# Performance work log

Hardware: AMD Instinct MI355X
Metric: run time of the kernel (lower is better)

The kernel has to match this reference:

```python
import jax, jax.numpy as jnp
import numpy as np

N_HEAD = 16


def setup_inputs() -> dict:
    key = jax.random.key(0)
    k0, k1, k2, k3 = jax.random.split(key, 4)
    B, T, C = 2, 2048, 1024
    scale = 0.02
    x = jax.random.normal(k0, (B, T, C), dtype=jnp.float32)
    W_attn = jax.random.normal(k1, (C, 3 * C), dtype=jnp.float32) * scale
    b_attn = jnp.zeros((3 * C,), dtype=jnp.float32)
    W_proj = jax.random.normal(k2, (C, C), dtype=jnp.float32) * scale
    b_proj = jnp.zeros((C,), dtype=jnp.float32)
    return {"x": x, "W_attn": W_attn, "b_attn": b_attn, "W_proj": W_proj, "b_proj": b_proj}


def reference(x, W_attn, b_attn, W_proj, b_proj):
    B, T, C = x.shape
    H = N_HEAD
    hd = C // H
    # fused qkv projection
    qkv = x @ W_attn + b_attn                      # [B, T, 3C]
    q, k, v = jnp.split(qkv, 3, axis=-1)
    q = q.reshape(B, T, H, hd).transpose(0, 2, 1, 3)  # [B, H, T, hd]
    k = k.reshape(B, T, H, hd).transpose(0, 2, 1, 3)
    v = v.reshape(B, T, H, hd).transpose(0, 2, 1, 3)
    # scaled dot-product attention with causal mask (past_kv=None -> seq_len == T)
    att = jnp.einsum('bhqd,bhkd->bhqk', q, k) / jnp.sqrt(jnp.float32(hd))
    causal = jnp.tril(jnp.ones((T, T), dtype=bool))  # [T, T]
    att = jnp.where(causal[None, None, :, :], att, jnp.float32(-jnp.inf))
    att = jax.nn.softmax(att, axis=-1)
    y = jnp.einsum('bhqk,bhkd->bhqd', att, v)        # [B, H, T, hd]
    y = y.transpose(0, 2, 1, 3).reshape(B, T, C)
    y = y @ W_proj + b_proj
    return (y, k, v)  # (output, present_k, present_v)
```

## Files before the change

kernel.cpp:

```cpp
#include <hip/hip_runtime.h>
#include <hip/hip_bf16.h>

typedef __bf16 bf16;
typedef __bf16 bf16x8 __attribute__((ext_vector_type(8)));
typedef float f32x4 __attribute__((ext_vector_type(4)));
typedef unsigned int u32;

#define MFMA_BF16(a, b, c) __builtin_amdgcn_mfma_f32_16x16x32_bf16((a), (b), (c), 0, 0, 0)

#define SEQ_T 2048
#define DIM_C 1024

__device__ inline void gload16(const void* g, void* l) {
  __builtin_amdgcn_global_load_lds((const __attribute__((address_space(1))) u32*)g,
                                   (__attribute__((address_space(3))) u32*)l, 16, 0, 0);
}

__device__ inline bf16x8 cvt8f(const f32x4 a, const f32x4 b) {
  bf16x8 r;
  r[0] = (bf16)a[0]; r[1] = (bf16)a[1]; r[2] = (bf16)a[2]; r[3] = (bf16)a[3];
  r[4] = (bf16)b[0]; r[5] = (bf16)b[1]; r[6] = (bf16)b[2]; r[7] = (bf16)b[3];
  return r;
}

__global__ __launch_bounds__(256) void prep_kernel(
    const float* __restrict__ x, const float* __restrict__ Wa,
    const float* __restrict__ Wp, bf16* __restrict__ xbf,
    bf16* __restrict__ wat, bf16* __restrict__ wpt) {
  const int tid = threadIdx.x;
  const int bid = blockIdx.x;
  if (bid < 2048) {
    const size_t i = ((size_t)bid * 256 + tid) * 8;
    *(bf16x8*)(xbf + i) = cvt8f(*(const f32x4*)(x + i), *(const f32x4*)(x + i + 4));
  } else if (bid < 3584) {
    const int cid = (bid - 2048) * 256 + tid;
    const int kg = cid / 3072, n = cid - kg * 3072;
    bf16x8 r;
#pragma unroll
    for (int j = 0; j < 8; j++) r[j] = (bf16)Wa[(size_t)(kg * 8 + j) * 3072 + n];
    *(bf16x8*)(wat + (size_t)cid * 8) = r;
  } else {
    const int cid = (bid - 3584) * 256 + tid;
    const int kg = cid >> 10, n = cid & 1023;
    bf16x8 r;
#pragma unroll
    for (int j = 0; j < 8; j++) r[j] = (bf16)Wp[(size_t)(kg * 8 + j) * 1024 + n];
    *(bf16x8*)(wpt + (size_t)cid * 8) = r;
  }
}

__global__ __launch_bounds__(256) void img_kernel(
    const float* __restrict__ K, const float* __restrict__ V,
    bf16* __restrict__ kimg, bf16* __restrict__ vimg) {
  const int gid = blockIdx.x * 256 + threadIdx.x;
  const int ka = gid >> 3, h8 = gid & 7;
  const size_t src = (size_t)ka * 64 + h8 * 8;
  const bf16x8 rk = cvt8f(*(const f32x4*)(K + src), *(const f32x4*)(K + src + 4));
  const bf16x8 rv = cvt8f(*(const f32x4*)(V + src), *(const f32x4*)(V + src + 4));
  const size_t tb = (size_t)(ka & ~63) * 64;
  const int kl = ka & 63, k7 = ka & 7, cq = (ka >> 3) & 7;
  *(bf16x8*)(kimg + tb + kl * 64 + ((h8 ^ k7) * 8)) = rk;
#pragma unroll
  for (int e = 0; e < 8; e++) {
    const int hr = h8 * 8 + e;
    vimg[tb + hr * 64 + ((cq ^ (hr & 7)) * 8) + k7] = rv[e];
  }
}

template <int MODE, int BM, int BK>
__global__ __launch_bounds__(256) void gemm_kernel(
    const bf16* __restrict__ A, const bf16* __restrict__ Wt,
    const float* __restrict__ bias, float* __restrict__ out0,
    float* __restrict__ out1, bf16* __restrict__ bq, int M, int N, int K) {
  constexpr int MI = BM / 32;
  constexpr int CA = BM * BK / 2048;
  constexpr int CB = BK / 16;
  constexpr int RPC = 512 / BK;
  constexpr int EPB = BK / 8;
  __shared__ bf16 As[2][BM * BK];
  __shared__ bf16 Bt[2][128 * BK];

  const int tid = threadIdx.x;
  const int wid = tid >> 6, lane = tid & 63;
  const int quad = lane >> 4, l16 = lane & 15;
  const int wm = (wid >> 1) * (BM / 2), wn = (wid & 1) * 64;
  const int m0 = blockIdx.y * BM, n0 = blockIdx.x * 128;
  const int lr = lane / EPB, lks = lane % EPB;

  const f32x4 zero = {0.f, 0.f, 0.f, 0.f};
  f32x4 acc[MI][4];
#pragma unroll
  for (int i = 0; i < MI; i++)
#pragma unroll
    for (int j = 0; j < 4; j++) acc[i][j] = zero;

  auto stage = [&](int buf, int kk) {
#pragma unroll
    for (int p = 0; p < CA; p++) {
      const int c = wid * CA + p;
      gload16(A + (size_t)(m0 + c * RPC + lr) * K + kk + lks * 8,
              (bf16*)As[buf] + c * 512);
    }
#pragma unroll
    for (int p = 0; p < CB; p++) {
      const int c = wid * CB + p;
      gload16(Wt + ((size_t)((kk >> 3) + lks) * N + n0 + c * RPC + lr) * 8,
              (bf16*)Bt[buf] + c * 512);
    }
  };

  const int nt = K / BK;
  stage(0, 0);
  __syncthreads();
  int cur = 0;
  for (int t = 0; t < nt; t++) {
    if (t + 1 < nt) stage(cur ^ 1, (t + 1) * BK);
#pragma unroll
    for (int kb = 0; kb < BK / 32; kb++) {
      bf16x8 af[MI], bfr[4];
#pragma unroll
      for (int i = 0; i < MI; i++)
        af[i] = *(const bf16x8*)&As[cur][(wm + i * 16 + l16) * BK + kb * 32 + quad * 8];
#pragma unroll
      for (int j = 0; j < 4; j++)
        bfr[j] = *(const bf16x8*)&Bt[cur][(wn + j * 16 + l16) * BK + kb * 32 + quad * 8];
#pragma unroll
      for (int i = 0; i < MI; i++)
#pragma unroll
        for (int j = 0; j < 4; j++)
          acc[i][j] = MFMA_BF16(af[i], bfr[j], acc[i][j]);
    }
    __syncthreads();
    cur ^= 1;
  }

#pragma unroll
  for (int i = 0; i < MI; i++) {
#pragma unroll
    for (int j = 0; j < 4; j++) {
      const int col = n0 + wn + j * 16 + l16;
      const float bv = bias[col];
#pragma unroll
      for (int r = 0; r < 4; r++) {
        const int gm = m0 + wm + i * 16 + quad * 4 + r;
        const float v = acc[i][j][r] + bv;
        if (MODE == 0) {
          out0[(size_t)gm * N + col] = v;
        } else {
          const int which = col >> 10, c = col & 1023;
          const int h = c >> 6, d = c & 63;
          const int b = gm >> 11, t = gm & (SEQ_T - 1);
          const size_t idx = ((size_t)(b * 16 + h) * SEQ_T + t) * 64 + d;
          if (which == 0) {
            bq[idx] = (bf16)(v * 0.18033688f);
          } else if (which == 1) {
            out0[idx] = v;
          } else {
            out1[idx] = v;
          }
        }
      }
    }
  }
}

__global__ __launch_bounds__(512) void attn_kernel(
    const bf16* __restrict__ Qbf, const bf16* __restrict__ Kimg,
    const bf16* __restrict__ Vimg, bf16* __restrict__ Y) {
  __shared__ bf16 Ks[2][4096];
  __shared__ bf16 Vt[2][4096];
  __shared__ bf16 Ps[8 * 1024];

  const int tid = threadIdx.x;
  const int wid = tid >> 6, lane = tid & 63;
  const int quad = lane >> 4, l16 = lane & 15;

  const int qt = (blockIdx.y < 16) ? ((int)gridDim.x - 1 - (int)blockIdx.x)
                                   : (int)blockIdx.x;
  const int bh = blockIdx.y;
  const int q0 = qt * 128;
  const int b = bh >> 4, h = bh & 15;

  const bf16* qp = Qbf + (size_t)bh * SEQ_T * 64;
  const bf16* kp = Kimg + (size_t)bh * SEQ_T * 64;
  const bf16* vp = Vimg + (size_t)bh * SEQ_T * 64;

  bf16x8 aq[2];
#pragma unroll
  for (int ks = 0; ks < 2; ks++)
    aq[ks] = *(const bf16x8*)(qp + (size_t)(q0 + wid * 16 + l16) * 64 + ks * 32 + quad * 8);

  bf16x8 bones;
#pragma unroll
  for (int j = 0; j < 8; j++) bones[j] = (bf16)1.0f;

  const f32x4 zero = {0.f, 0.f, 0.f, 0.f};
  f32x4 oacc[4], lacc;
  lacc = zero;
#pragma unroll
  for (int t = 0; t < 4; t++) oacc[t] = zero;

  const int last = 2 * qt + 1;

  auto stage = [&](int buf, int t) {
    const size_t tb = (size_t)t * 4096 + (size_t)tid * 8;
    bf16* wb = &Ks[buf][wid << 9];
    gload16(kp + tb, wb);
    gload16(vp + tb, &Vt[buf][wid << 9]);
  };

  stage(0, 0);
  __syncthreads();

  for (int it = 0; it <= last; ++it) {
    const int cur = it & 1;
    if (it < last) stage(cur ^ 1, it + 1);

    const bool skip = (it == last) && (wid < 4);
    const bool dm = (it == 2 * qt && wid < 4) || (it == last && wid >= 4);

    if (!skip) {
      f32x4 sa[4];
#pragma unroll
      for (int nt = 0; nt < 4; nt++) {
        const int row = nt * 16 + l16, r7 = l16 & 7;
        const bf16x8 bk0 = *(const bf16x8*)&Ks[cur][row * 64 + ((quad ^ r7) * 8)];
        const bf16x8 bk1 = *(const bf16x8*)&Ks[cur][row * 64 + (((quad + 4) ^ r7) * 8)];
        f32x4 s = MFMA_BF16(aq[0], bk0, zero);
        sa[nt] = MFMA_BF16(aq[1], bk1, s);
      }
      if (dm) {
#pragma unroll
        for (int nt = 0; nt < 4; nt++) {
          const int col = it * 64 + nt * 16 + l16;
#pragma unroll
          for (int r = 0; r < 4; r++) {
            const int row = q0 + wid * 16 + quad * 4 + r;
            if (col > row) sa[nt][r] = -1e30f;
          }
        }
      }
      bf16* pwb = &Ps[wid * 1024];
#pragma unroll
      for (int nt = 0; nt < 4; nt++) {
#pragma unroll
        for (int r = 0; r < 4; r++) {
          const int pr = quad * 4 + r;
          pwb[pr * 64 + (((2 * nt + (l16 >> 3)) ^ (pr & 7)) * 8) + (l16 & 7)] =
              (bf16)exp2f(sa[nt][r]);
        }
      }
      bf16x8 ap[2];
#pragma unroll
      for (int ks = 0; ks < 2; ks++)
        ap[ks] = *(const bf16x8*)&pwb[l16 * 64 + (((ks * 4 + quad) ^ (l16 & 7)) * 8)];
      lacc = MFMA_BF16(ap[0], bones, lacc);
      lacc = MFMA_BF16(ap[1], bones, lacc);
#pragma unroll
      for (int nt = 0; nt < 4; nt++) {
        const int hr = nt * 16 + l16, h7 = l16 & 7;
#pragma unroll
        for (int ks = 0; ks < 2; ks++) {
          const bf16x8 bv = *(const bf16x8*)&Vt[cur][hr * 64 + (((ks * 4 + quad) ^ h7) * 8)];
          oacc[nt] = MFMA_BF16(ap[ks], bv, oacc[nt]);
        }
      }
    }
    __syncthreads();
  }

  float inv[4];
#pragma unroll
  for (int r = 0; r < 4; r++) inv[r] = 1.f / lacc[r];
#pragma unroll
  for (int nt = 0; nt < 4; nt++) {
#pragma unroll
    for (int r = 0; r < 4; r++) {
      const int row = q0 + wid * 16 + quad * 4 + r;
      const int col = h * 64 + nt * 16 + l16;
      Y[((size_t)(b * SEQ_T + row)) * DIM_C + col] = (bf16)(oacc[nt][r] * inv[r]);
    }
  }
}

extern "C" void kernel_launch(void* const* d_in, const int* in_sizes, int n_in,
                              void* d_out, int out_size, void* d_ws, size_t ws_size,
                              hipStream_t stream) {
  (void)in_sizes; (void)n_in; (void)out_size; (void)ws_size;
  const float* x = (const float*)d_in[0];
  const float* W_attn = (const float*)d_in[1];
  const float* b_attn = (const float*)d_in[2];
  const float* W_proj = (const float*)d_in[3];
  const float* b_proj = (const float*)d_in[4];

  float* out = (float*)d_out;
  float* y_out = out;
  float* k_out = out + (size_t)4194304;
  float* v_out = out + (size_t)8388608;
  bf16* qbf = (bf16*)d_out;
  bf16* kimg = (bf16*)d_out + 4194304;
  bf16* y_att = (bf16*)d_in[0];
  bf16* vimg = (bf16*)d_in[0] + 4194304;
  bf16* xbf = (bf16*)d_ws;
  bf16* wat = xbf + 4194304;
  bf16* wpt = wat + 3145728;

  prep_kernel<<<4096, 256, 0, stream>>>(x, W_attn, W_proj, xbf, wat, wpt);
  gemm_kernel<1, 128, 32><<<dim3(3072 / 128, 4096 / 128), 256, 0, stream>>>(
      xbf, wat, b_attn, k_out, v_out, qbf, 4096, 3072, 1024);
  img_kernel<<<2048, 256, 0, stream>>>(k_out, v_out, kimg, vimg);
  attn_kernel<<<dim3(SEQ_T / 128, 32), 512, 0, stream>>>(qbf, kimg, vimg, y_att);
  gemm_kernel<0, 64, 64><<<dim3(1024 / 128, 4096 / 64), 256, 0, stream>>>(
      y_att, wpt, b_proj, y_out, nullptr, nullptr, 4096, 1024, 1024);
}
```

Before: 207.2 us.

## Use atomic work queue for attention and transpose V through LDS

The attention kernel becomes persistent. Each block pulls (query-tile, head) jobs from a global atomic counter, ordered longest causal tile first, to balance the uneven causal workload across CUs. The img kernel now resets the counter and splits into two parts: V blocks build the transposed, swizzled tile in shared memory and then write it out coalesced, and K blocks keep the old path. This adds an atomic and a barrier per job and reuses the workspace head as the counter.

```diff
diff --git a/kernel.cpp b/kernel.cpp
--- a/kernel.cpp
+++ b/kernel.cpp
@@ -51,19 +51,36 @@
 
 __global__ __launch_bounds__(256) void img_kernel(
     const float* __restrict__ K, const float* __restrict__ V,
-    bf16* __restrict__ kimg, bf16* __restrict__ vimg) {
-  const int gid = blockIdx.x * 256 + threadIdx.x;
-  const int ka = gid >> 3, h8 = gid & 7;
-  const size_t src = (size_t)ka * 64 + h8 * 8;
-  const bf16x8 rk = cvt8f(*(const f32x4*)(K + src), *(const f32x4*)(K + src + 4));
-  const bf16x8 rv = cvt8f(*(const f32x4*)(V + src), *(const f32x4*)(V + src + 4));
-  const size_t tb = (size_t)(ka & ~63) * 64;
-  const int kl = ka & 63, k7 = ka & 7, cq = (ka >> 3) & 7;
-  *(bf16x8*)(kimg + tb + kl * 64 + ((h8 ^ k7) * 8)) = rk;
-#pragma unroll
-  for (int e = 0; e < 8; e++) {
-    const int hr = h8 * 8 + e;
-    vimg[tb + hr * 64 + ((cq ^ (hr & 7)) * 8) + k7] = rv[e];
+    bf16* __restrict__ kimg, bf16* __restrict__ vimg, int* __restrict__ cnt) {
+  const int tid = threadIdx.x;
+  const int bid = blockIdx.x;
+  if (bid == 0 && tid == 0) *cnt = 0;
+  if (bid < 1024) {
+    __shared__ bf16 vt[4096];
+    const size_t tb = (size_t)bid * 4096;
+    const int key = tid >> 2, cs = (tid & 3) * 16;
+    const int k7 = key & 7, cq = (key >> 3) & 7;
+    const float* vsrc = V + tb + (size_t)key * 64 + cs;
+#pragma unroll
+    for (int jj = 0; jj < 16; jj += 4) {
+      const f32x4 v4 = *(const f32x4*)(vsrc + jj);
+#pragma unroll
+      for (int e = 0; e < 4; e++) {
+        const int hr = cs + jj + e;
+        vt[hr * 64 + ((cq ^ (hr & 7)) * 8) + k7] = (bf16)v4[e];
+      }
+    }
+    __syncthreads();
+    *(bf16x8*)(vimg + tb + tid * 16) = *(const bf16x8*)&vt[tid * 16];
+    *(bf16x8*)(vimg + tb + tid * 16 + 8) = *(const bf16x8*)&vt[tid * 16 + 8];
+  } else {
+    const int gid = (bid - 1024) * 256 + tid;
+    const int ka = gid >> 3, h8 = gid & 7;
+    const size_t src = (size_t)ka * 64 + h8 * 8;
+    const bf16x8 rk = cvt8f(*(const f32x4*)(K + src), *(const f32x4*)(K + src + 4));
+    const size_t tb = (size_t)(ka & ~63) * 64;
+    const int kl = ka & 63, k7 = ka & 7;
+    *(bf16x8*)(kimg + tb + kl * 64 + ((h8 ^ k7) * 8)) = rk;
   }
 }
 
@@ -166,119 +183,123 @@
 
 __global__ __launch_bounds__(512) void attn_kernel(
     const bf16* __restrict__ Qbf, const bf16* __restrict__ Kimg,
-    const bf16* __restrict__ Vimg, bf16* __restrict__ Y) {
+    const bf16* __restrict__ Vimg, bf16* __restrict__ Y, int* __restrict__ cnt) {
   __shared__ bf16 Ks[2][4096];
   __shared__ bf16 Vt[2][4096];
   __shared__ bf16 Ps[8 * 1024];
+  __shared__ int js;
 
   const int tid = threadIdx.x;
   const int wid = tid >> 6, lane = tid & 63;
   const int quad = lane >> 4, l16 = lane & 15;
 
-  const int qt = (blockIdx.y < 16) ? ((int)gridDim.x - 1 - (int)blockIdx.x)
-                                   : (int)blockIdx.x;
-  const int bh = blockIdx.y;
-  const int q0 = qt * 128;
-  const int b = bh >> 4, h = bh & 15;
-
-  const bf16* qp = Qbf + (size_t)bh * SEQ_T * 64;
-  const bf16* kp = Kimg + (size_t)bh * SEQ_T * 64;
-  const bf16* vp = Vimg + (size_t)bh * SEQ_T * 64;
-
-  bf16x8 aq[2];
-#pragma unroll
-  for (int ks = 0; ks < 2; ks++)
-    aq[ks] = *(const bf16x8*)(qp + (size_t)(q0 + wid * 16 + l16) * 64 + ks * 32 + quad * 8);
-
   bf16x8 bones;
 #pragma unroll
   for (int j = 0; j < 8; j++) bones[j] = (bf16)1.0f;
-
   const f32x4 zero = {0.f, 0.f, 0.f, 0.f};
-  f32x4 oacc[4], lacc;
-  lacc = zero;
-#pragma unroll
-  for (int t = 0; t < 4; t++) oacc[t] = zero;
-
-  const int last = 2 * qt + 1;
-
-  auto stage = [&](int buf, int t) {
-    const size_t tb = (size_t)t * 4096 + (size_t)tid * 8;
-    bf16* wb = &Ks[buf][wid << 9];
-    gload16(kp + tb, wb);
-    gload16(vp + tb, &Vt[buf][wid << 9]);
-  };
-
-  stage(0, 0);
-  __syncthreads();
-
-  for (int it = 0; it <= last; ++it) {
-    const int cur = it & 1;
-    if (it < last) stage(cur ^ 1, it + 1);
-
-    const bool skip = (it == last) && (wid < 4);
-    const bool dm = (it == 2 * qt && wid < 4) || (it == last && wid >= 4);
-
-    if (!skip) {
-      f32x4 sa[4];
-#pragma unroll
-      for (int nt = 0; nt < 4; nt++) {
-        const int row = nt * 16 + l16, r7 = l16 & 7;
-        const bf16x8 bk0 = *(const bf16x8*)&Ks[cur][row * 64 + ((quad ^ r7) * 8)];
-        const bf16x8 bk1 = *(const bf16x8*)&Ks[cur][row * 64 + (((quad + 4) ^ r7) * 8)];
-        f32x4 s = MFMA_BF16(aq[0], bk0, zero);
-        sa[nt] = MFMA_BF16(aq[1], bk1, s);
+
+  for (;;) {
+    if (tid == 0) js = atomicAdd(cnt, 1);
+    __syncthreads();
+    const int j = js;
+    if (j >= 512) break;
+    const int qt = 15 - (j >> 5), bh = j & 31;
+    const int q0 = qt * 128;
+    const int b = bh >> 4, h = bh & 15;
+
+    const bf16* qp = Qbf + (size_t)bh * SEQ_T * 64;
+    const bf16* kp = Kimg + (size_t)bh * SEQ_T * 64;
+    const bf16* vp = Vimg + (size_t)bh * SEQ_T * 64;
+
+    bf16x8 aq[2];
+#pragma unroll
+    for (int ks = 0; ks < 2; ks++)
+      aq[ks] = *(const bf16x8*)(qp + (size_t)(q0 + wid * 16 + l16) * 64 + ks * 32 + quad * 8);
+
+    f32x4 oacc[4], lacc;
+    lacc = zero;
+#pragma unroll
+    for (int t = 0; t < 4; t++) oacc[t] = zero;
+
+    const int last = 2 * qt + 1;
+
+    auto stage = [&](int buf, int t) {
+      const size_t tb = (size_t)t * 4096 + (size_t)tid * 8;
+      gload16(kp + tb, &Ks[buf][wid << 9]);
+      gload16(vp + tb, &Vt[buf][wid << 9]);
+    };
+
+    stage(0, 0);
+    __syncthreads();
+
+    for (int it = 0; it <= last; ++it) {
+      const int cur = it & 1;
+      if (it < last) stage(cur ^ 1, it + 1);
+
+      const bool skip = (it == last) && (wid < 4);
+      const bool dm = (it == 2 * qt && wid < 4) || (it == last && wid >= 4);
+
+      if (!skip) {
+        f32x4 sa[4];
+#pragma unroll
+        for (int nt = 0; nt < 4; nt++) {
+          const int row = nt * 16 + l16, r7 = l16 & 7;
+          const bf16x8 bk0 = *(const bf16x8*)&Ks[cur][row * 64 + ((quad ^ r7) * 8)];
+          const bf16x8 bk1 = *(const bf16x8*)&Ks[cur][row * 64 + (((quad + 4) ^ r7) * 8)];
+          f32x4 s = MFMA_BF16(aq[0], bk0, zero);
+          sa[nt] = MFMA_BF16(aq[1], bk1, s);
+        }
+        if (dm) {
+#pragma unroll
+          for (int nt = 0; nt < 4; nt++) {
+            const int col = it * 64 + nt * 16 + l16;
+#pragma unroll
+            for (int r = 0; r < 4; r++) {
+              const int row = q0 + wid * 16 + quad * 4 + r;
+              if (col > row) sa[nt][r] = -1e30f;
+            }
+          }
+        }
+        bf16* pwb = &Ps[wid * 1024];
+#pragma unroll
+        for (int nt = 0; nt < 4; nt++) {
+#pragma unroll
+          for (int r = 0; r < 4; r++) {
+            const int pr = quad * 4 + r;
+            pwb[pr * 64 + (((2 * nt + (l16 >> 3)) ^ (pr & 7)) * 8) + (l16 & 7)] =
+                (bf16)exp2f(sa[nt][r]);
+          }
+        }
+        bf16x8 ap[2];
+#pragma unroll
+        for (int ks = 0; ks < 2; ks++)
+          ap[ks] = *(const bf16x8*)&pwb[l16 * 64 + (((ks * 4 + quad) ^ (l16 & 7)) * 8)];
+        lacc = MFMA_BF16(ap[0], bones, lacc);
+        lacc = MFMA_BF16(ap[1], bones, lacc);
+#pragma unroll
+        for (int nt = 0; nt < 4; nt++) {
+          const int hr = nt * 16 + l16, h7 = l16 & 7;
+#pragma unroll
+          for (int ks = 0; ks < 2; ks++) {
+            const bf16x8 bv = *(const bf16x8*)&Vt[cur][hr * 64 + (((ks * 4 + quad) ^ h7) * 8)];
+            oacc[nt] = MFMA_BF16(ap[ks], bv, oacc[nt]);
+          }
+        }
       }
-      if (dm) {
-#pragma unroll
-        for (int nt = 0; nt < 4; nt++) {
-          const int col = it * 64 + nt * 16 + l16;
-#pragma unroll
-          for (int r = 0; r < 4; r++) {
-            const int row = q0 + wid * 16 + quad * 4 + r;
-            if (col > row) sa[nt][r] = -1e30f;
-          }
-        }
+      __syncthreads();
+    }
+
+    float inv[4];
+#pragma unroll
+    for (int r = 0; r < 4; r++) inv[r] = 1.f / lacc[r];
+#pragma unroll
+    for (int nt = 0; nt < 4; nt++) {
+#pragma unroll
+      for (int r = 0; r < 4; r++) {
+        const int row = q0 + wid * 16 + quad * 4 + r;
+        const int col = h * 64 + nt * 16 + l16;
+        Y[((size_t)(b * SEQ_T + row)) * DIM_C + col] = (bf16)(oacc[nt][r] * inv[r]);
       }
-      bf16* pwb = &Ps[wid * 1024];
-#pragma unroll
-      for (int nt = 0; nt < 4; nt++) {
-#pragma unroll
-        for (int r = 0; r < 4; r++) {
-          const int pr = quad * 4 + r;
-          pwb[pr * 64 + (((2 * nt + (l16 >> 3)) ^ (pr & 7)) * 8) + (l16 & 7)] =
-              (bf16)exp2f(sa[nt][r]);
-        }
-      }
-      bf16x8 ap[2];
-#pragma unroll
-      for (int ks = 0; ks < 2; ks++)
-        ap[ks] = *(const bf16x8*)&pwb[l16 * 64 + (((ks * 4 + quad) ^ (l16 & 7)) * 8)];
-      lacc = MFMA_BF16(ap[0], bones, lacc);
-      lacc = MFMA_BF16(ap[1], bones, lacc);
-#pragma unroll
-      for (int nt = 0; nt < 4; nt++) {
-        const int hr = nt * 16 + l16, h7 = l16 & 7;
-#pragma unroll
-        for (int ks = 0; ks < 2; ks++) {
-          const bf16x8 bv = *(const bf16x8*)&Vt[cur][hr * 64 + (((ks * 4 + quad) ^ h7) * 8)];
-          oacc[nt] = MFMA_BF16(ap[ks], bv, oacc[nt]);
-        }
-      }
-    }
-    __syncthreads();
-  }
-
-  float inv[4];
-#pragma unroll
-  for (int r = 0; r < 4; r++) inv[r] = 1.f / lacc[r];
-#pragma unroll
-  for (int nt = 0; nt < 4; nt++) {
-#pragma unroll
-    for (int r = 0; r < 4; r++) {
-      const int row = q0 + wid * 16 + quad * 4 + r;
-      const int col = h * 64 + nt * 16 + l16;
-      Y[((size_t)(b * SEQ_T + row)) * DIM_C + col] = (bf16)(oacc[nt][r] * inv[r]);
     }
   }
 }
@@ -304,12 +325,13 @@
   bf16* xbf = (bf16*)d_ws;
   bf16* wat = xbf + 4194304;
   bf16* wpt = wat + 3145728;
+  int* cnt = (int*)d_ws;
 
   prep_kernel<<<4096, 256, 0, stream>>>(x, W_attn, W_proj, xbf, wat, wpt);
   gemm_kernel<1, 128, 32><<<dim3(3072 / 128, 4096 / 128), 256, 0, stream>>>(
       xbf, wat, b_attn, k_out, v_out, qbf, 4096, 3072, 1024);
-  img_kernel<<<2048, 256, 0, stream>>>(k_out, v_out, kimg, vimg);
-  attn_kernel<<<dim3(SEQ_T / 128, 32), 512, 0, stream>>>(qbf, kimg, vimg, y_att);
+  img_kernel<<<3072, 256, 0, stream>>>(k_out, v_out, kimg, vimg, cnt);
+  attn_kernel<<<768, 512, 0, stream>>>(qbf, kimg, vimg, y_att, cnt);
   gemm_kernel<0, 64, 64><<<dim3(1024 / 128, 4096 / 64), 256, 0, stream>>>(
       y_att, wpt, b_proj, y_out, nullptr, nullptr, 4096, 1024, 1024);
 }
```

Result: slower. 211.9 us (+2.3%).
